# Kernel tuning notes

Hardware: AMD Instinct MI355X
Metric: run time of the kernel (lower is better)

## Reference

```python
import jax, jax.numpy as jnp
import numpy as np

VOCAB = 50257
DIM = 768


def setup_inputs() -> dict:
    key = jax.random.key(0)
    W = jax.random.normal(key, (VOCAB, DIM), dtype=jnp.float32)
    return {"W": W, "batch_size": 8192}


def reference(W, batch_size):
    # batch_size only controls tiling in the torch original; math is tile-independent.
    V, d = W.shape
    eps = jnp.finfo(W.dtype).eps  # torch F.rms_norm default eps
    # RMS-normalize each row: wn = w / sqrt(mean(w^2) + eps)
    Wn = W * jax.lax.rsqrt(jnp.mean(W * W, axis=-1, keepdims=True) + eps)
    # sum_{i,j} (wn_i . wn_j)^2 = ||Wn^T Wn||_F^2  (d x d Gram trick, avoids V x V matrix)
    G = jnp.einsum('vd,ve->de', Wn, Wn)  # [d, d]
    total_sq = jnp.sum(G * G)
    # diagonal terms (i == j): (||wn_i||^2)^2
    diag = jnp.sum(Wn * Wn, axis=-1)  # [V]
    diag_sq = jnp.sum(diag * diag)
    # strict upper triangle = (all pairs - diagonal) / 2
    upper_sum = (total_sq - diag_sq) * 0.5
    n_pairs = V * (V - 1) / 2
    return upper_sum / n_pairs
```

## Files before the change

kernel.cpp:

```cpp
#include <hip/hip_runtime.h>
#include <hip/hip_bf16.h>
#include <stdint.h>


#define V_ROWS 50257
#define DIM 768
#define VPAD 50304
#define NIT 786
#define SPLITS 24
#define CHUNK 33
#define NT 6
#define NTILES 21
#define EPS 1.1920928955078125e-07f

#define WT_OFF  262144ull
#define P_OFF   (262144ull + 77266944ull)

typedef __attribute__((ext_vector_type(8))) short bf16x8;
typedef __attribute__((ext_vector_type(4))) float f32x4;

__device__ __forceinline__ void gload_lds16(const void* g, void* l) {
    __builtin_amdgcn_global_load_lds(
        (const __attribute__((address_space(1))) void*)(g),
        (__attribute__((address_space(3))) void*)(l), 16, 0, 0);
}

__global__ void k0_zero(double* acc) {
    if (threadIdx.x < 2) acc[threadIdx.x] = 0.0;
}

__global__ __launch_bounds__(256) void k12_norm_transpose(const float* __restrict__ W,
                                                          __hip_bfloat16* __restrict__ WT,
                                                          double* __restrict__ acc) {
    __shared__ float rv_s[64];
    __shared__ double part[4];
    __shared__ __hip_bfloat16 lds2[64][64];
    const int v0 = blockIdx.x * 64;
    const int tid = threadIdx.x;
    const int w = tid >> 6, lane = tid & 63;

    const int prow = tid >> 2;
    const int q = tid & 3;
    const int vv1 = v0 + prow;
    float s = 0.f;
    if (vv1 < V_ROWS) {
        const float4* rp = (const float4*)(W + (size_t)vv1 * DIM);
        #pragma unroll
        for (int j = 0; j < 48; ++j) {
            float4 x = rp[q + j * 4];
            s += x.x * x.x + x.y * x.y + x.z * x.z + x.w * x.w;
        }
    }
    s += __shfl_xor(s, 1);
    s += __shfl_xor(s, 2);
    const float rv = (vv1 < V_ROWS) ? 1.0f / sqrtf(s * (1.0f / DIM) + EPS) : 0.f;
    if (q == 0) rv_s[prow] = rv;
    double d = 0.0;
    if (q == 0 && vv1 < V_ROWS) {
        float dg = s * rv * rv;
        d = (double)dg * (double)dg;
    }
    #pragma unroll
    for (int off = 32; off >= 4; off >>= 1) d += __shfl_down(d, off);
    if (lane == 0) part[w] = d;
    __syncthreads();
    if (tid == 0) atomicAdd(&acc[0], part[0] + part[1] + part[2] + part[3]);

    const int rowg = tid >> 4;
    const int cq = tid & 15;
    const int ksw = cq & 7;
    const int cl = tid >> 3;
    const int ch = tid & 7;
    const int rk = ((ch ^ ((cl >> 2) & 7)) << 3);
    #pragma unroll 1
    for (int ct = 0; ct < 12; ++ct) {
        const int c0 = ct * 64;
        __syncthreads();
        #pragma unroll
        for (int rr = 0; rr < 4; ++rr) {
            const int row = rr * 16 + rowg;
            const int vv = v0 + row;
            float4 x = make_float4(0.f, 0.f, 0.f, 0.f);
            const float rvv = rv_s[row];
            if (vv < V_ROWS)
                x = *(const float4*)(W + (size_t)vv * DIM + c0 + cq * 4);
            const int p = row ^ (ksw << 3);
            lds2[cq * 4 + 0][p] = __float2bfloat16(x.x * rvv);
            lds2[cq * 4 + 1][p] = __float2bfloat16(x.y * rvv);
            lds2[cq * 4 + 2][p] = __float2bfloat16(x.z * rvv);
            lds2[cq * 4 + 3][p] = __float2bfloat16(x.w * rvv);
        }
        __syncthreads();
        #pragma unroll
        for (int half = 0; half < 2; ++half) {
            const int c = cl + half * 32;
            float4 val = *(const float4*)(&lds2[c][rk]);
            *(float4*)(WT + (size_t)(c0 + c) * VPAD + v0 + ch * 8) = val;
        }
    }
}

__global__ __launch_bounds__(256) void k3_gram(const unsigned short* __restrict__ WT,
                                               float* __restrict__ P) {
    __shared__ unsigned short lsA[128 * 64];
    __shared__ unsigned short lsB[128 * 64];
    const int bx = blockIdx.x;
    const int t = bx / SPLITS, s = bx % SPLITS;
    int tt = t, ti = 0, rem = NT;
    while (tt >= rem) { tt -= rem; --rem; ++ti; }
    const int tj = ti + tt;
    const int I = ti * 128, J = tj * 128;
    const int i0 = s * CHUNK;
    const int i1 = min(NIT, i0 + CHUNK);

    const int tid = threadIdx.x, lane = tid & 63, w = tid >> 6;
    const int wr = w >> 1, wc = w & 1;
    const int r16 = lane & 15, kq = lane >> 4;

    int srow[4], sblk[4], sbase[4];
    #pragma unroll
    for (int p = 0; p < 4; ++p) {
        const int base = (p * 4 + w) * 1024;
        const int o = base + lane * 16;
        srow[p] = o >> 7;
        sblk[p] = ((o >> 4) & 7) ^ (srow[p] & 7);
        sbase[p] = base >> 1;
    }

    int ia[4][2], ib[4][2];
    #pragma unroll
    for (int m = 0; m < 4; ++m) {
        const int ra = wr * 64 + m * 16 + r16;
        const int rb = wc * 64 + m * 16 + r16;
        #pragma unroll
        for (int kf = 0; kf < 2; ++kf) {
            ia[m][kf] = ra * 64 + (((kf * 4 + kq) ^ (ra & 7)) * 8);
            ib[m][kf] = rb * 64 + (((kf * 4 + kq) ^ (rb & 7)) * 8);
        }
    }

    f32x4 acc[4][4] = {};

    for (int it = i0; it < i1; ++it) {
        const int kv = it * 64;
        __syncthreads();
        #pragma unroll
        for (int p = 0; p < 4; ++p) {
            const unsigned short* ga = WT + (size_t)(I + srow[p]) * VPAD + kv + sblk[p] * 8;
            gload_lds16(ga, &lsA[sbase[p]]);
            const unsigned short* gb = WT + (size_t)(J + srow[p]) * VPAD + kv + sblk[p] * 8;
            gload_lds16(gb, &lsB[sbase[p]]);
        }
        __syncthreads();
        bf16x8 af[4][2], bfr[4][2];
        #pragma unroll
        for (int m = 0; m < 4; ++m) {
            #pragma unroll
            for (int kf = 0; kf < 2; ++kf) {
                af[m][kf]  = *(const bf16x8*)(&lsA[ia[m][kf]]);
                bfr[m][kf] = *(const bf16x8*)(&lsB[ib[m][kf]]);
            }
        }
        #pragma unroll
        for (int kf = 0; kf < 2; ++kf)
            #pragma unroll
            for (int m = 0; m < 4; ++m)
                #pragma unroll
                for (int n = 0; n < 4; ++n)
                    acc[m][n] = __builtin_amdgcn_mfma_f32_16x16x32_bf16(
                        af[m][kf], bfr[n][kf], acc[m][n], 0, 0, 0);
    }

    float* Pw = P + (size_t)bx * (128 * 128);
    #pragma unroll
    for (int m = 0; m < 4; ++m)
        #pragma unroll
        for (int n = 0; n < 4; ++n)
            #pragma unroll
            for (int j = 0; j < 4; ++j) {
                const int rr = wr * 64 + m * 16 + kq * 4 + j;
                const int cc = wc * 64 + n * 16 + r16;
                Pw[rr * 128 + cc] = acc[m][n][j];
            }
}

__global__ __launch_bounds__(256) void k4_reduce(const float* __restrict__ P,
                                                 double* __restrict__ acc) {
    __shared__ double part[4];
    const int t = blockIdx.x, seg = blockIdx.y;
    int tt = t, ti = 0, rem = NT;
    while (tt >= rem) { tt -= rem; --rem; ++ti; }
    const int tj = ti + tt;
    const double wt = (ti == tj) ? 1.0 : 2.0;
    const int tid = threadIdx.x;
    double local = 0.0;
    for (int e = seg * 2048 + tid; e < (seg + 1) * 2048; e += 256) {
        float ssum = 0.f;
        #pragma unroll
        for (int s = 0; s < SPLITS; ++s)
            ssum += P[(size_t)(t * SPLITS + s) * 16384 + e];
        local += (double)ssum * (double)ssum;
    }
    #pragma unroll
    for (int off = 32; off; off >>= 1) local += __shfl_down(local, off);
    if ((tid & 63) == 0) part[tid >> 6] = local;
    __syncthreads();
    if (tid == 0) atomicAdd(&acc[1], (part[0] + part[1] + part[2] + part[3]) * wt);
}

__global__ void k5_final(const double* __restrict__ acc, float* __restrict__ out) {
    const double n_pairs = (double)V_ROWS * (double)(V_ROWS - 1) * 0.5;
    out[0] = (float)((acc[1] - acc[0]) * 0.5 / n_pairs);
}

extern "C" void kernel_launch(void* const* d_in, const int* in_sizes, int n_in,
                              void* d_out, int out_size, void* d_ws, size_t ws_size,
                              hipStream_t stream) {
    const float* W = (const float*)d_in[0];
    char* ws = (char*)d_ws;
    double* acc = (double*)ws;
    __hip_bfloat16* WT = (__hip_bfloat16*)(ws + WT_OFF);
    float* P = (float*)(ws + P_OFF);

    hipLaunchKernelGGL(k0_zero, dim3(1), dim3(64), 0, stream, acc);
    hipLaunchKernelGGL(k12_norm_transpose, dim3(VPAD / 64), dim3(256), 0, stream,
                       W, WT, acc);
    hipLaunchKernelGGL(k3_gram, dim3(NTILES * SPLITS), dim3(256), 0, stream,
                       (const unsigned short*)WT, P);
    hipLaunchKernelGGL(k4_reduce, dim3(NTILES, 8), dim3(256), 0, stream, P, acc);
    hipLaunchKernelGGL(k5_final, dim3(1), dim3(1), 0, stream, acc, (float*)d_out);
}
```

Baseline: 312.2 us.

## Split norm/transpose kernel into parallel passes and remap gram blocks per XCD

The fused norm-plus-transpose kernel becomes two kernels. One computes the per-row RMS scale and the diagonal sum into a workspace buffer. The other does the normalized bf16 transpose over a 2D grid with one 64x64 tile per block, replacing the serial 12-step column loop. Separately, the gram kernel remaps block indices so that each XCD gets a contiguous range of tile/split work, which is meant to improve L2 reuse of shared WT rows. The cost is an extra launch and a small round trip of the row scales through global memory.

New measurement: 344.8 us. 1.1x slower.

```diff
diff --git a/kernel.cpp b/kernel.cpp
--- a/kernel.cpp
+++ b/kernel.cpp
@@ -13,6 +13,7 @@
 #define NTILES 21
 #define EPS 1.1920928955078125e-07f
 
+#define R_OFF   256ull
 #define WT_OFF  262144ull
 #define P_OFF   (262144ull + 77266944ull)
 
@@ -29,74 +30,74 @@
     if (threadIdx.x < 2) acc[threadIdx.x] = 0.0;
 }
 
-__global__ __launch_bounds__(256) void k12_norm_transpose(const float* __restrict__ W,
-                                                          __hip_bfloat16* __restrict__ WT,
-                                                          double* __restrict__ acc) {
+__global__ __launch_bounds__(256) void k1_norms(const float* __restrict__ W,
+                                                float* __restrict__ r,
+                                                double* __restrict__ acc) {
+    __shared__ double part[4];
+    const int tid = threadIdx.x;
+    const int l32 = tid & 31;
+    const int v = blockIdx.x * 8 + (tid >> 5);
+    float s = 0.f;
+    if (v < V_ROWS) {
+        const float4* rp = (const float4*)(W + (size_t)v * DIM);
+        #pragma unroll
+        for (int j = 0; j < 6; ++j) {
+            float4 x = rp[l32 + j * 32];
+            s += x.x * x.x + x.y * x.y + x.z * x.z + x.w * x.w;
+        }
+    }
+    #pragma unroll
+    for (int off = 16; off; off >>= 1) s += __shfl_xor(s, off);
+    double d = 0.0;
+    if (l32 == 0) {
+        float rv = 0.f;
+        if (v < V_ROWS) {
+            rv = 1.0f / sqrtf(s * (1.0f / DIM) + EPS);
+            float dg = s * rv * rv;
+            d = (double)dg * (double)dg;
+        }
+        r[v] = rv;
+    }
+    d += __shfl_down(d, 32);
+    if ((tid & 63) == 0) part[tid >> 6] = d;
+    __syncthreads();
+    if (tid == 0) atomicAdd(&acc[0], part[0] + part[1] + part[2] + part[3]);
+}
+
+__global__ __launch_bounds__(256) void k2_transpose(const float* __restrict__ W,
+                                                    const float* __restrict__ r,
+                                                    __hip_bfloat16* __restrict__ WT) {
     __shared__ float rv_s[64];
-    __shared__ double part[4];
     __shared__ __hip_bfloat16 lds2[64][64];
     const int v0 = blockIdx.x * 64;
+    const int c0 = blockIdx.y * 64;
     const int tid = threadIdx.x;
-    const int w = tid >> 6, lane = tid & 63;
-
-    const int prow = tid >> 2;
-    const int q = tid & 3;
-    const int vv1 = v0 + prow;
-    float s = 0.f;
-    if (vv1 < V_ROWS) {
-        const float4* rp = (const float4*)(W + (size_t)vv1 * DIM);
-        #pragma unroll
-        for (int j = 0; j < 48; ++j) {
-            float4 x = rp[q + j * 4];
-            s += x.x * x.x + x.y * x.y + x.z * x.z + x.w * x.w;
-        }
-    }
-    s += __shfl_xor(s, 1);
-    s += __shfl_xor(s, 2);
-    const float rv = (vv1 < V_ROWS) ? 1.0f / sqrtf(s * (1.0f / DIM) + EPS) : 0.f;
-    if (q == 0) rv_s[prow] = rv;
-    double d = 0.0;
-    if (q == 0 && vv1 < V_ROWS) {
-        float dg = s * rv * rv;
-        d = (double)dg * (double)dg;
-    }
-    #pragma unroll
-    for (int off = 32; off >= 4; off >>= 1) d += __shfl_down(d, off);
-    if (lane == 0) part[w] = d;
-    __syncthreads();
-    if (tid == 0) atomicAdd(&acc[0], part[0] + part[1] + part[2] + part[3]);
-
-    const int rowg = tid >> 4;
-    const int cq = tid & 15;
+    if (tid < 64) rv_s[tid] = r[v0 + tid];
+    __syncthreads();
+    const int rowg = tid >> 4, cq = tid & 15;
     const int ksw = cq & 7;
-    const int cl = tid >> 3;
-    const int ch = tid & 7;
+    #pragma unroll
+    for (int rr = 0; rr < 4; ++rr) {
+        const int row = rr * 16 + rowg;
+        const int vv = v0 + row;
+        float4 x = make_float4(0.f, 0.f, 0.f, 0.f);
+        const float rvv = rv_s[row];
+        if (vv < V_ROWS)
+            x = *(const float4*)(W + (size_t)vv * DIM + c0 + cq * 4);
+        const int p = row ^ (ksw << 3);
+        lds2[cq * 4 + 0][p] = __float2bfloat16(x.x * rvv);
+        lds2[cq * 4 + 1][p] = __float2bfloat16(x.y * rvv);
+        lds2[cq * 4 + 2][p] = __float2bfloat16(x.z * rvv);
+        lds2[cq * 4 + 3][p] = __float2bfloat16(x.w * rvv);
+    }
+    __syncthreads();
+    const int cl = tid >> 3, ch = tid & 7;
     const int rk = ((ch ^ ((cl >> 2) & 7)) << 3);
-    #pragma unroll 1
-    for (int ct = 0; ct < 12; ++ct) {
-        const int c0 = ct * 64;
-        __syncthreads();
-        #pragma unroll
-        for (int rr = 0; rr < 4; ++rr) {
-            const int row = rr * 16 + rowg;
-            const int vv = v0 + row;
-            float4 x = make_float4(0.f, 0.f, 0.f, 0.f);
-            const float rvv = rv_s[row];
-            if (vv < V_ROWS)
-                x = *(const float4*)(W + (size_t)vv * DIM + c0 + cq * 4);
-            const int p = row ^ (ksw << 3);
-            lds2[cq * 4 + 0][p] = __float2bfloat16(x.x * rvv);
-            lds2[cq * 4 + 1][p] = __float2bfloat16(x.y * rvv);
-            lds2[cq * 4 + 2][p] = __float2bfloat16(x.z * rvv);
-            lds2[cq * 4 + 3][p] = __float2bfloat16(x.w * rvv);
-        }
-        __syncthreads();
-        #pragma unroll
-        for (int half = 0; half < 2; ++half) {
-            const int c = cl + half * 32;
-            float4 val = *(const float4*)(&lds2[c][rk]);
-            *(float4*)(WT + (size_t)(c0 + c) * VPAD + v0 + ch * 8) = val;
-        }
+    #pragma unroll
+    for (int half = 0; half < 2; ++half) {
+        const int c = cl + half * 32;
+        float4 val = *(const float4*)(&lds2[c][rk]);
+        *(float4*)(WT + (size_t)(c0 + c) * VPAD + v0 + ch * 8) = val;
     }
 }
 
@@ -104,7 +105,8 @@
                                                float* __restrict__ P) {
     __shared__ unsigned short lsA[128 * 64];
     __shared__ unsigned short lsB[128 * 64];
-    const int bx = blockIdx.x;
+    const int bid = blockIdx.x;
+    const int bx = (bid & 7) * (NTILES * SPLITS / 8) + (bid >> 3);
     const int t = bx / SPLITS, s = bx % SPLITS;
     int tt = t, ti = 0, rem = NT;
     while (tt >= rem) { tt -= rem; --rem; ++ti; }
@@ -219,12 +221,14 @@
     const float* W = (const float*)d_in[0];
     char* ws = (char*)d_ws;
     double* acc = (double*)ws;
+    float* r = (float*)(ws + R_OFF);
     __hip_bfloat16* WT = (__hip_bfloat16*)(ws + WT_OFF);
     float* P = (float*)(ws + P_OFF);
 
     hipLaunchKernelGGL(k0_zero, dim3(1), dim3(64), 0, stream, acc);
-    hipLaunchKernelGGL(k12_norm_transpose, dim3(VPAD / 64), dim3(256), 0, stream,
-                       W, WT, acc);
+    hipLaunchKernelGGL(k1_norms, dim3(VPAD / 8), dim3(256), 0, stream, W, r, acc);
+    hipLaunchKernelGGL(k2_transpose, dim3(VPAD / 64, DIM / 64), dim3(256), 0, stream,
+                       W, r, WT);
     hipLaunchKernelGGL(k3_gram, dim3(NTILES * SPLITS), dim3(256), 0, stream,
                        (const unsigned short*)WT, P);
     hipLaunchKernelGGL(k4_reduce, dim3(NTILES, 8), dim3(256), 0, stream, P, acc);
```
